# Kernel tuning notes

Measured on AMD Instinct MI355X. Metric: run time of the kernel, lower is better.

The kernel has to match this reference:

```python
import jax, jax.numpy as jnp
import numpy as np

B, L, E, H, EXP = 2, 2048, 1024, 16, 4
D = E // H
EPS = 1e-5

def layernorm(x, g, b):
    mu = jnp.mean(x, axis=-1, keepdims=True)
    var = jnp.var(x, axis=-1, keepdims=True)
    return (x - mu) * jax.lax.rsqrt(var + EPS) * g + b

def setup_inputs() -> dict:
    key = jax.random.key(0)
    ks = jax.random.split(key, 12)
    s = 0.02
    return {
        "x": jax.random.normal(ks[0], (B, L, E), dtype=jnp.float32),
        "ln1_g": jnp.ones((E,), jnp.float32),
        "ln1_b": jnp.zeros((E,), jnp.float32),
        "W_qkv": jax.random.normal(ks[1], (E, 3 * E), dtype=jnp.float32) * s,
        "W_proj": jax.random.normal(ks[2], (E, E), dtype=jnp.float32) * s,
        "b_proj": jnp.zeros((E,), jnp.float32),
        "ln2_g": jnp.ones((E,), jnp.float32),
        "ln2_b": jnp.zeros((E,), jnp.float32),
        "W1": jax.random.normal(ks[3], (E, EXP * E), dtype=jnp.float32) * s,
        "b1": jnp.zeros((EXP * E,), jnp.float32),
        "W2": jax.random.normal(ks[4], (EXP * E, E), dtype=jnp.float32) * s,
        "b2": jnp.zeros((E,), jnp.float32),
    }

def reference(x, ln1_g, ln1_b, W_qkv, W_proj, b_proj, ln2_g, ln2_b, W1, b1, W2, b2):
    # --- attention sub-block (pre-LN) ---
    h = layernorm(x, ln1_g, ln1_b)                      # [B,L,E]
    qkv = h @ W_qkv                                      # [B,L,3E]
    q, k, v = jnp.split(qkv, 3, axis=-1)
    q = q.reshape(B, L, H, D).transpose(0, 2, 1, 3)      # [B,H,L,D]
    k = k.reshape(B, L, H, D).transpose(0, 2, 1, 3)
    v = v.reshape(B, L, H, D).transpose(0, 2, 1, 3)
    scale = jnp.sqrt(jnp.float32(E))                     # NOTE: module divides by sqrt(E), not sqrt(D)
    att = jnp.einsum('bhqd,bhkd->bhqk', q, k) / scale
    att = jax.nn.softmax(att, axis=-1)
    out = jnp.einsum('bhqk,bhkd->bhqd', att, v)          # [B,H,L,D]
    out = out.transpose(0, 2, 1, 3).reshape(B, L, E)
    x = x + out @ W_proj + b_proj                         # residual
    # --- feed-forward sub-block (pre-LN) ---
    h = layernorm(x, ln2_g, ln2_b)
    h = jax.nn.gelu(h @ W1 + b1, approximate=False)       # torch GELU is exact erf
    x = x + h @ W2 + b2
    return x
```

## Files before the change

### kernel.cpp

```cpp
#include <hip/hip_runtime.h>
#include <cstdint>
#include <cstddef>


typedef __bf16 bht;
typedef __attribute__((ext_vector_type(8))) __bf16 bf16x8;
typedef __attribute__((ext_vector_type(4))) __bf16 bf16x4;
typedef __attribute__((ext_vector_type(4))) float f32x4;
typedef __attribute__((ext_vector_type(4))) short short4v;

#define B_ 2
#define L_ 2048
#define E_ 1024
#define H_ 16
#define D_ 64
#define ROWS_ (B_ * L_)

#define QSCALE_ 0.045084441f

__device__ __forceinline__ void glds16(const void* g, void* l) {
    __builtin_amdgcn_global_load_lds(
        (const __attribute__((address_space(1))) unsigned int*)g,
        (__attribute__((address_space(3))) unsigned int*)l, 16, 0, 0);
}

__device__ __forceinline__ short4v as_s4(bf16x4 v) {
    return __builtin_bit_cast(short4v, v);
}

__global__ __launch_bounds__(256)
void transpose_cast(const float* __restrict__ in, bht* __restrict__ out, int R, int C) {
    __shared__ float tile[32][33];
    const int bx = blockIdx.x * 32;
    const int by = blockIdx.y * 32;
    const int tx = threadIdx.x, ty = threadIdx.y;
    #pragma unroll
    for (int i = 0; i < 32; i += 8)
        tile[ty + i][tx] = in[(size_t)(by + ty + i) * C + bx + tx];
    __syncthreads();
    #pragma unroll
    for (int i = 0; i < 32; i += 8)
        out[(size_t)(bx + ty + i) * R + by + tx] = (bht)tile[tx][ty + i];
}

__global__ __launch_bounds__(256)
void ln_kernel(const float* __restrict__ x, const float* __restrict__ g,
               const float* __restrict__ b, bht* __restrict__ out) {
    const int row = blockIdx.x, t = threadIdx.x;
    const float4 v = ((const float4*)(x + (size_t)row * E_))[t];
    float s  = v.x + v.y + v.z + v.w;
    float ss = v.x*v.x + v.y*v.y + v.z*v.z + v.w*v.w;
    #pragma unroll
    for (int off = 32; off > 0; off >>= 1) {
        s  += __shfl_down(s, off);
        ss += __shfl_down(ss, off);
    }
    __shared__ float red[8];
    const int wave = t >> 6, lane = t & 63;
    if (lane == 0) { red[wave] = s; red[4 + wave] = ss; }
    __syncthreads();
    s  = red[0] + red[1] + red[2] + red[3];
    ss = red[4] + red[5] + red[6] + red[7];
    const float mean = s * (1.0f / (float)E_);
    const float var  = ss * (1.0f / (float)E_) - mean * mean;
    const float rstd = rsqrtf(var + 1e-5f);
    const float4 gv = ((const float4*)g)[t];
    const float4 bv = ((const float4*)b)[t];
    bf16x4 o;
    o.x = (bht)((v.x - mean) * rstd * gv.x + bv.x);
    o.y = (bht)((v.y - mean) * rstd * gv.y + bv.y);
    o.z = (bht)((v.z - mean) * rstd * gv.z + bv.z);
    o.w = (bht)((v.w - mean) * rstd * gv.w + bv.w);
    *(bf16x4*)(out + (size_t)row * E_ + t * 4) = o;
}

enum { EPI_QKV = 0, EPI_RESID = 1, EPI_GELU = 2 };

template <int EPI>
__global__ __launch_bounds__(256)
void gemm_bt(const bht* __restrict__ A, const bht* __restrict__ Bt,
             const float* __restrict__ bias, const float* __restrict__ resid,
             void* __restrict__ outp,
             bht* __restrict__ qo, bht* __restrict__ ko, bht* __restrict__ vto,
             int M, int N, int K) {
    __shared__ __align__(16) char smem[33792];
    bht* As = (bht*)smem;
    bht* Bs = (bht*)(smem + 16384);
    const int t = threadIdx.x;
    const int lane = t & 63, wave = t >> 6;
    const int lane15 = lane & 15, quad = lane >> 4;
    const int waveM = wave >> 1, waveN = wave & 1;
    const int bm = blockIdx.y * 128, bn = blockIdx.x * 128;

    f32x4 acc[4][4];
    #pragma unroll
    for (int i = 0; i < 4; ++i)
        #pragma unroll
        for (int j = 0; j < 4; ++j)
            acc[i][j] = f32x4{0.f, 0.f, 0.f, 0.f};

    const int swz = lane15 & 7;

    for (int k0 = 0; k0 < K; k0 += 64) {
        #pragma unroll
        for (int i = 0; i < 4; ++i) {
            const int g = i * 256 + t;
            const int row = g >> 3;
            const int col = ((g & 7) ^ (row & 7)) * 8;
            glds16(A  + (size_t)(bm + row) * K + k0 + col, (char*)As + (size_t)g * 16);
            glds16(Bt + (size_t)(bn + row) * K + k0 + col, (char*)Bs + (size_t)g * 16);
        }
        __syncthreads();
        #pragma unroll
        for (int kk = 0; kk < 2; ++kk) {
            const int pc = ((kk * 4 + quad) ^ swz) * 8;
            bf16x8 af[4], bfv[4];
            #pragma unroll
            for (int i = 0; i < 4; ++i)
                af[i] = *(const bf16x8*)(As + (waveM * 64 + i * 16 + lane15) * 64 + pc);
            #pragma unroll
            for (int j = 0; j < 4; ++j)
                bfv[j] = *(const bf16x8*)(Bs + (waveN * 64 + j * 16 + lane15) * 64 + pc);
            #pragma unroll
            for (int i = 0; i < 4; ++i)
                #pragma unroll
                for (int j = 0; j < 4; ++j)
                    acc[i][j] = __builtin_amdgcn_mfma_f32_16x16x32_bf16(af[i], bfv[j], acc[i][j], 0, 0, 0);
        }
        __syncthreads();
    }

    if constexpr (EPI == EPI_QKV) {
        if (bn >= 2048) {
            bht* Vtile = (bht*)smem;
            #pragma unroll
            for (int i = 0; i < 4; ++i) {
                const int rl0 = waveM * 64 + i * 16 + quad * 4;
                #pragma unroll
                for (int j = 0; j < 4; ++j) {
                    const int cl = waveN * 64 + j * 16 + lane15;
                    #pragma unroll
                    for (int r = 0; r < 4; ++r)
                        Vtile[(size_t)cl * 132 + rl0 + r] = (bht)acc[i][j][r];
                }
            }
            __syncthreads();
            const int b = bm >> 11;
            const int l0 = bm & 2047;
            #pragma unroll
            for (int it = 0; it < 8; ++it) {
                const int row = it * 16 + (t >> 4);
                const int ch  = t & 15;
                const int cg = (bn - 2048) + row;
                const int h = cg >> 6, d = cg & 63;
                const int bh = b * H_ + h;
                bf16x8 vv = *(const bf16x8*)(Vtile + (size_t)row * 132 + ch * 8);
                if (t & 128)
                    vv = __builtin_shufflevector(vv, vv, 4, 5, 6, 7, 0, 1, 2, 3);
                *(bf16x8*)(vto + ((size_t)bh * D_ + d) * L_ + l0 + ch * 8) = vv;
            }
        } else {
            #pragma unroll
            for (int i = 0; i < 4; ++i) {
                const int row0 = bm + waveM * 64 + i * 16 + quad * 4;
                #pragma unroll
                for (int j = 0; j < 4; ++j) {
                    const int col = bn + waveN * 64 + j * 16 + lane15;
                    const int seg = col >> 10;
                    const int c = col & 1023;
                    const int h = c >> 6, d = c & 63;
                    #pragma unroll
                    for (int r = 0; r < 4; ++r) {
                        const int m = row0 + r;
                        const int b = m >> 11, l = m & 2047;
                        const int bh = b * H_ + h;
                        const float v = acc[i][j][r];
                        if (seg == 0)
                            qo[((size_t)bh * L_ + l) * D_ + d] = (bht)(v * QSCALE_);
                        else
                            ko[((size_t)bh * L_ + l) * D_ + d] = (bht)v;
                    }
                }
            }
        }
    } else {
        #pragma unroll
        for (int i = 0; i < 4; ++i) {
            const int row0 = bm + waveM * 64 + i * 16 + quad * 4;
            #pragma unroll
            for (int j = 0; j < 4; ++j) {
                const int col = bn + waveN * 64 + j * 16 + lane15;
                #pragma unroll
                for (int r = 0; r < 4; ++r) {
                    const int m = row0 + r;
                    float v = acc[i][j][r];
                    if (EPI == EPI_RESID) {
                        ((float*)outp)[(size_t)m * N + col] =
                            v + bias[col] + resid[(size_t)m * N + col];
                    } else {
                        v += bias[col];
                        v = 0.5f * v * (1.0f + erff(v * 0.70710678118654752f));
                        ((bht*)outp)[(size_t)m * N + col] = (bht)v;
                    }
                }
            }
        }
    }
}

template <int EPI>
__global__ __launch_bounds__(256)
void gemm_bt64(const bht* __restrict__ A, const bht* __restrict__ Bt,
               const float* __restrict__ bias, const float* __restrict__ resid,
               void* __restrict__ outp, int M, int N, int K) {
    __shared__ __align__(16) bht As[64 * 64];
    __shared__ __align__(16) bht Bs[128 * 64];
    const int t = threadIdx.x;
    const int lane = t & 63, wave = t >> 6;
    const int lane15 = lane & 15, quad = lane >> 4;
    const int waveM = wave >> 1, waveN = wave & 1;
    const int bm = blockIdx.y * 64, bn = blockIdx.x * 128;

    f32x4 acc[2][4];
    #pragma unroll
    for (int i = 0; i < 2; ++i)
        #pragma unroll
        for (int j = 0; j < 4; ++j)
            acc[i][j] = f32x4{0.f, 0.f, 0.f, 0.f};

    const int swz = lane15 & 7;

    for (int k0 = 0; k0 < K; k0 += 64) {
        #pragma unroll
        for (int i = 0; i < 2; ++i) {
            const int g = i * 256 + t;
            const int row = g >> 3;
            const int col = ((g & 7) ^ (row & 7)) * 8;
            glds16(A + (size_t)(bm + row) * K + k0 + col, (char*)As + (size_t)g * 16);
        }
        #pragma unroll
        for (int i = 0; i < 4; ++i) {
            const int g = i * 256 + t;
            const int row = g >> 3;
            const int col = ((g & 7) ^ (row & 7)) * 8;
            glds16(Bt + (size_t)(bn + row) * K + k0 + col, (char*)Bs + (size_t)g * 16);
        }
        __syncthreads();
        #pragma unroll
        for (int kk = 0; kk < 2; ++kk) {
            const int pc = ((kk * 4 + quad) ^ swz) * 8;
            bf16x8 af[2], bfv[4];
            #pragma unroll
            for (int i = 0; i < 2; ++i)
                af[i] = *(const bf16x8*)(As + (waveM * 32 + i * 16 + lane15) * 64 + pc);
            #pragma unroll
            for (int j = 0; j < 4; ++j)
                bfv[j] = *(const bf16x8*)(Bs + (waveN * 64 + j * 16 + lane15) * 64 + pc);
            #pragma unroll
            for (int i = 0; i < 2; ++i)
                #pragma unroll
                for (int j = 0; j < 4; ++j)
                    acc[i][j] = __builtin_amdgcn_mfma_f32_16x16x32_bf16(af[i], bfv[j], acc[i][j], 0, 0, 0);
        }
        __syncthreads();
    }

    #pragma unroll
    for (int i = 0; i < 2; ++i) {
        const int row0 = bm + waveM * 32 + i * 16 + quad * 4;
        #pragma unroll
        for (int j = 0; j < 4; ++j) {
            const int col = bn + waveN * 64 + j * 16 + lane15;
            #pragma unroll
            for (int r = 0; r < 4; ++r) {
                const int m = row0 + r;
                float v = acc[i][j][r];
                if (EPI == EPI_RESID) {
                    ((float*)outp)[(size_t)m * N + col] =
                        v + bias[col] + resid[(size_t)m * N + col];
                } else {
                    v += bias[col];
                    v = 0.5f * v * (1.0f + erff(v * 0.70710678118654752f));
                    ((bht*)outp)[(size_t)m * N + col] = (bht)v;
                }
            }
        }
    }
}

#define KT_ 128
#define NT_ (L_ / KT_)

__global__ __launch_bounds__(256)
void attn_kernel(const bht* __restrict__ Q, const bht* __restrict__ Kb,
                 const bht* __restrict__ Vt, bht* __restrict__ O) {
    __shared__ __align__(16) bht Ks[KT_ * 64];
    __shared__ __align__(16) bht Vs[64 * KT_];
    __shared__ float Ls[4][16];
    const int t = threadIdx.x;
    const int lane = t & 63, wave = t >> 6;
    const int lane15 = lane & 15, quad = lane >> 4;
    const int bh = blockIdx.x, qt = blockIdx.y;

    const bht* Qh = Q  + (size_t)bh * L_ * D_;
    const bht* Kh = Kb + (size_t)bh * L_ * D_;
    const bht* Vh = Vt + (size_t)bh * D_ * L_;

    const int q0 = qt * 64 + wave * 16;

    bf16x8 aq[2];
    #pragma unroll
    for (int kc = 0; kc < 2; ++kc)
        aq[kc] = *(const bf16x8*)(Qh + (size_t)(q0 + lane15) * D_ + kc * 32 + quad * 8);

    f32x4 o_acc[4];
    #pragma unroll
    for (int db = 0; db < 4; ++db) o_acc[db] = f32x4{0.f, 0.f, 0.f, 0.f};
    float l_sum = 0.f;

    const int pc0 = (quad ^ (lane15 & 7)) * 8;
    const int pc1 = pc0 ^ 32;
    const int vhalf4 = ((quad & 1) ^ ((lane15 >> 3) & 1)) * 4;

    auto stageK = [&](int kt2) {
        const int key0 = kt2 * KT_;
        #pragma unroll
        for (int i = 0; i < 4; ++i) {
            const int g = i * 256 + t;
            const int krow = g >> 3;
            const int ksc = ((g & 7) ^ (krow & 7)) * 8;
            glds16(Kh + (size_t)(key0 + krow) * D_ + ksc, (char*)Ks + (size_t)g * 16);
        }
    };
    auto stageV = [&](int kt2) {
        const int key0 = kt2 * KT_;
        #pragma unroll
        for (int i = 0; i < 4; ++i) {
            const int g = i * 256 + t;
            const int vrow = g >> 4;
            const int vsc = ((g & 15) ^ (vrow & 7)) * 8;
            glds16(Vh + (size_t)vrow * L_ + key0 + vsc, (char*)Vs + (size_t)g * 16);
        }
    };

    stageK(0);
    stageV(0);

    for (int kt = 0; kt < NT_; ++kt) {
        asm volatile("s_waitcnt vmcnt(4) lgkmcnt(0)" ::: "memory");
        __builtin_amdgcn_s_barrier();

        __builtin_amdgcn_s_setprio(1);
        short4v pk[8];
        #pragma unroll
        for (int nb = 0; nb < 8; ++nb) {
            const bf16x8 ak0 = *(const bf16x8*)(Ks + (nb * 16 + lane15) * 64 + pc0);
            const bf16x8 ak1 = *(const bf16x8*)(Ks + (nb * 16 + lane15) * 64 + pc1);
            f32x4 st = __builtin_amdgcn_mfma_f32_16x16x32_bf16(
                ak0, aq[0], f32x4{0.f, 0.f, 0.f, 0.f}, 0, 0, 0);
            st = __builtin_amdgcn_mfma_f32_16x16x32_bf16(ak1, aq[1], st, 0, 0, 0);
            bf16x4 pkv;
            #pragma unroll
            for (int r = 0; r < 4; ++r) {
                const float pv = exp2f(st[r]);
                l_sum += pv;
                pkv[r] = (bht)pv;
            }
            pk[nb] = as_s4(pkv);
        }
        __builtin_amdgcn_s_setprio(0);

        asm volatile("s_waitcnt vmcnt(0) lgkmcnt(0)" ::: "memory");
        __builtin_amdgcn_s_barrier();
        if (kt + 1 < NT_) stageK(kt + 1);

        __builtin_amdgcn_s_setprio(1);
        #pragma unroll
        for (int nb = 0; nb < 8; ++nb) {
            #pragma unroll
            for (int db = 0; db < 4; ++db) {
                const int row = db * 16 + lane15;
                const int c16 = (nb * 2 + (quad >> 1)) ^ (row & 7);
                const bf16x4 bv = *(const bf16x4*)(Vs + row * KT_ + c16 * 8 + vhalf4);
                o_acc[db] = __builtin_amdgcn_mfma_f32_16x16x16bf16_1k(
                    pk[nb], as_s4(bv), o_acc[db], 0, 0, 0);
            }
        }
        __builtin_amdgcn_s_setprio(0);

        asm volatile("s_waitcnt lgkmcnt(0)" ::: "memory");
        __builtin_amdgcn_s_barrier();
        if (kt + 1 < NT_) stageV(kt + 1);
    }

    l_sum += __shfl_xor(l_sum, 16);
    l_sum += __shfl_xor(l_sum, 32);
    Ls[wave][lane15] = l_sum;
    asm volatile("s_waitcnt lgkmcnt(0)" ::: "memory");

    const int b = bh >> 4, h = bh & 15;
    #pragma unroll
    for (int r = 0; r < 4; ++r) {
        const int l = q0 + quad * 4 + r;
        const float inv = 1.0f / Ls[wave][quad * 4 + r];
        #pragma unroll
        for (int db = 0; db < 4; ++db)
            O[((size_t)b * L_ + l) * E_ + h * 64 + db * 16 + lane15] =
                (bht)(o_acc[db][r] * inv);
    }
}

extern "C" void kernel_launch(void* const* d_in, const int* in_sizes, int n_in,
                              void* d_out, int out_size, void* d_ws, size_t ws_size,
                              hipStream_t stream) {
    const float* x      = (const float*)d_in[0];
    const float* ln1_g  = (const float*)d_in[1];
    const float* ln1_b  = (const float*)d_in[2];
    const float* W_qkv  = (const float*)d_in[3];
    const float* W_proj = (const float*)d_in[4];
    const float* b_proj = (const float*)d_in[5];
    const float* ln2_g  = (const float*)d_in[6];
    const float* ln2_b  = (const float*)d_in[7];
    const float* W1     = (const float*)d_in[8];
    const float* b1     = (const float*)d_in[9];
    const float* W2     = (const float*)d_in[10];
    const float* b2     = (const float*)d_in[11];
    float* out = (float*)d_out;

    char* ws = (char*)d_ws;
    auto alloc = [&](size_t bytes) {
        char* p = ws;
        ws += (bytes + 255) & ~(size_t)255;
        return p;
    };
    bht*   WqkvT  = (bht*)alloc((size_t)3072 * 1024 * 2);
    bht*   WprojT = (bht*)alloc((size_t)1024 * 1024 * 2);
    bht*   W1T    = (bht*)alloc((size_t)4096 * 1024 * 2);
    bht*   W2T    = (bht*)alloc((size_t)1024 * 4096 * 2);
    bht*   hb     = (bht*)alloc((size_t)ROWS_ * E_ * 2);
    float* x1     = (float*)alloc((size_t)ROWS_ * E_ * 4);
    bht*   Qb     = (bht*)alloc((size_t)B_ * H_ * L_ * D_ * 2);
    bht*   Kbuf   = (bht*)alloc((size_t)B_ * H_ * L_ * D_ * 2);
    bht*   Vtb    = (bht*)alloc((size_t)B_ * H_ * D_ * L_ * 2);
    bht*   attno  = (bht*)alloc((size_t)ROWS_ * E_ * 2);
    bht*   ffn1   = Qb;

    transpose_cast<<<dim3(3072 / 32, 1024 / 32), dim3(32, 8), 0, stream>>>(W_qkv, WqkvT, 1024, 3072);
    transpose_cast<<<dim3(1024 / 32, 1024 / 32), dim3(32, 8), 0, stream>>>(W_proj, WprojT, 1024, 1024);
    transpose_cast<<<dim3(4096 / 32, 1024 / 32), dim3(32, 8), 0, stream>>>(W1, W1T, 1024, 4096);
    transpose_cast<<<dim3(1024 / 32, 4096 / 32), dim3(32, 8), 0, stream>>>(W2, W2T, 4096, 1024);

    ln_kernel<<<ROWS_, 256, 0, stream>>>(x, ln1_g, ln1_b, hb);

    gemm_bt<EPI_QKV><<<dim3(3072 / 128, ROWS_ / 128), 256, 0, stream>>>(
        hb, WqkvT, nullptr, nullptr, nullptr, Qb, Kbuf, Vtb, ROWS_, 3072, 1024);

    attn_kernel<<<dim3(B_ * H_, L_ / 64), 256, 0, stream>>>(Qb, Kbuf, Vtb, attno);

    gemm_bt64<EPI_RESID><<<dim3(1024 / 128, ROWS_ / 64), 256, 0, stream>>>(
        attno, WprojT, b_proj, x, x1, ROWS_, 1024, 1024);

    ln_kernel<<<ROWS_, 256, 0, stream>>>(x1, ln2_g, ln2_b, hb);

    gemm_bt<EPI_GELU><<<dim3(4096 / 128, ROWS_ / 128), 256, 0, stream>>>(
        hb, W1T, b1, nullptr, ffn1, nullptr, nullptr, nullptr, ROWS_, 4096, 1024);

    gemm_bt64<EPI_RESID><<<dim3(1024 / 128, ROWS_ / 64), 256, 0, stream>>>(
        ffn1, W2T, b2, x1, out, ROWS_, 1024, 4096);

    (void)in_sizes; (void)n_in; (void)out_size; (void)ws_size;
}
```

Baseline: 382.0 us.

## Replace 128x128 GEMM with triple-buffered 256x256 tile kernel for QKV and FFN1

Replaces the single-buffered 128x128 bf16 GEMM used for the QKV projection and the first FFN layer with a 256x256-tile, 512-thread kernel. It triple-buffers LDS over 32-wide K steps and splits each step into two MFMA phases with staged loads in between. The goal is more operand reuse per byte loaded and overlap of global-to-LDS traffic with MFMA work. The V-transpose epilogue is redone in two halves so it fits the larger tile. Separately, attention swaps exp2f for the hardware exp2 builtin. The cost is higher register and LDS pressure, and fewer blocks on the grid (192 and 256).

Result: faster. 354.7 us (-7.1%).

```diff
diff --git a/kernel.cpp b/kernel.cpp
--- a/kernel.cpp
+++ b/kernel.cpp
@@ -26,6 +26,14 @@
 
 __device__ __forceinline__ short4v as_s4(bf16x4 v) {
     return __builtin_bit_cast(short4v, v);
+}
+
+__device__ __forceinline__ float fast_exp2(float x) {
+#if __has_builtin(__builtin_amdgcn_exp2f)
+    return __builtin_amdgcn_exp2f(x);
+#else
+    return exp2f(x);
+#endif
 }
 
 __global__ __launch_bounds__(256)
@@ -77,135 +85,178 @@
 enum { EPI_QKV = 0, EPI_RESID = 1, EPI_GELU = 2 };
 
 template <int EPI>
-__global__ __launch_bounds__(256)
-void gemm_bt(const bht* __restrict__ A, const bht* __restrict__ Bt,
-             const float* __restrict__ bias, const float* __restrict__ resid,
-             void* __restrict__ outp,
+__global__ __launch_bounds__(512, 2)
+void gemm256(const bht* __restrict__ A, const bht* __restrict__ Bt,
+             const float* __restrict__ bias, void* __restrict__ outp,
              bht* __restrict__ qo, bht* __restrict__ ko, bht* __restrict__ vto,
              int M, int N, int K) {
-    __shared__ __align__(16) char smem[33792];
-    bht* As = (bht*)smem;
-    bht* Bs = (bht*)(smem + 16384);
+    __shared__ __align__(16) char smem_[98304];
     const int t = threadIdx.x;
     const int lane = t & 63, wave = t >> 6;
     const int lane15 = lane & 15, quad = lane >> 4;
-    const int waveM = wave >> 1, waveN = wave & 1;
-    const int bm = blockIdx.y * 128, bn = blockIdx.x * 128;
-
-    f32x4 acc[4][4];
-    #pragma unroll
-    for (int i = 0; i < 4; ++i)
+    const int waveM = wave >> 2, waveN = wave & 3;
+    const int bm = blockIdx.y * 256, bn = blockIdx.x * 256;
+
+    f32x4 acc[8][4];
+    #pragma unroll
+    for (int i = 0; i < 8; ++i)
         #pragma unroll
         for (int j = 0; j < 4; ++j)
             acc[i][j] = f32x4{0.f, 0.f, 0.f, 0.f};
 
-    const int swz = lane15 & 7;
-
-    for (int k0 = 0; k0 < K; k0 += 64) {
-        #pragma unroll
-        for (int i = 0; i < 4; ++i) {
-            const int g = i * 256 + t;
-            const int row = g >> 3;
-            const int col = ((g & 7) ^ (row & 7)) * 8;
-            glds16(A  + (size_t)(bm + row) * K + k0 + col, (char*)As + (size_t)g * 16);
-            glds16(Bt + (size_t)(bn + row) * K + k0 + col, (char*)Bs + (size_t)g * 16);
-        }
-        __syncthreads();
-        #pragma unroll
-        for (int kk = 0; kk < 2; ++kk) {
-            const int pc = ((kk * 4 + quad) ^ swz) * 8;
-            bf16x8 af[4], bfv[4];
-            #pragma unroll
-            for (int i = 0; i < 4; ++i)
-                af[i] = *(const bf16x8*)(As + (waveM * 64 + i * 16 + lane15) * 64 + pc);
-            #pragma unroll
-            for (int j = 0; j < 4; ++j)
-                bfv[j] = *(const bf16x8*)(Bs + (waveN * 64 + j * 16 + lane15) * 64 + pc);
-            #pragma unroll
-            for (int i = 0; i < 4; ++i)
+    const int apc = ((quad ^ (lane15 & 3)) & 3) * 8;
+    const int aoff = waveM * 4096 + lane15 * 32 + apc;
+    const int boff = waveN * 2048 + lane15 * 32 + apc;
+
+    auto stage_step = [&](int s, int op, int bufi) {
+        const int k0 = s * 32;
+        const bht* src = op ? Bt : A;
+        const int rb = op ? bn : bm;
+        char* dst = smem_ + (size_t)bufi * 32768 + op * 16384;
+        #pragma unroll
+        for (int i = 0; i < 2; ++i) {
+            const int g = i * 512 + t;
+            const int row = g >> 2;
+            const int c = ((g & 3) ^ (row & 3)) * 8;
+            glds16(src + (size_t)(rb + row) * K + k0 + c, dst + (size_t)g * 16);
+        }
+    };
+
+    const int NT = K >> 5;
+    stage_step(0, 0, 0); stage_step(0, 1, 0);
+    stage_step(1, 0, 1); stage_step(1, 1, 1);
+
+    int cb = 0;
+    for (int s = 0; s < NT; ++s) {
+        const int nb2 = (cb >= 1) ? cb - 1 : 2;
+        if (s + 2 < NT) {
+            stage_step(s + 2, 0, nb2);
+            asm volatile("s_waitcnt vmcnt(6)" ::: "memory");
+        } else if (s + 1 < NT) {
+            asm volatile("s_waitcnt vmcnt(4)" ::: "memory");
+        } else {
+            asm volatile("s_waitcnt vmcnt(0)" ::: "memory");
+        }
+        __builtin_amdgcn_s_barrier();
+        asm volatile("" ::: "memory");
+
+        const bht* Au = (const bht*)(smem_ + (size_t)cb * 32768);
+        const bht* Bu = (const bht*)(smem_ + (size_t)cb * 32768 + 16384);
+        bf16x8 af0[4], bfv[4];
+        #pragma unroll
+        for (int m = 0; m < 4; ++m)
+            af0[m] = *(const bf16x8*)(Au + aoff + m * 512);
+        #pragma unroll
+        for (int n = 0; n < 4; ++n)
+            bfv[n] = *(const bf16x8*)(Bu + boff + n * 512);
+        asm volatile("s_waitcnt lgkmcnt(0)" ::: "memory");
+        __builtin_amdgcn_s_setprio(1);
+        #pragma unroll
+        for (int m = 0; m < 4; ++m)
+            #pragma unroll
+            for (int n = 0; n < 4; ++n)
+                acc[m][n] = __builtin_amdgcn_mfma_f32_16x16x32_bf16(af0[m], bfv[n], acc[m][n], 0, 0, 0);
+        __builtin_amdgcn_s_setprio(0);
+        __builtin_amdgcn_s_barrier();
+        asm volatile("" ::: "memory");
+
+        bf16x8 af1[4];
+        #pragma unroll
+        for (int m = 0; m < 4; ++m)
+            af1[m] = *(const bf16x8*)(Au + aoff + (m + 4) * 512);
+        if (s + 2 < NT) stage_step(s + 2, 1, nb2);
+        asm volatile("s_waitcnt lgkmcnt(0)" ::: "memory");
+        __builtin_amdgcn_s_setprio(1);
+        #pragma unroll
+        for (int m = 0; m < 4; ++m)
+            #pragma unroll
+            for (int n = 0; n < 4; ++n)
+                acc[m + 4][n] = __builtin_amdgcn_mfma_f32_16x16x32_bf16(af1[m], bfv[n], acc[m + 4][n], 0, 0, 0);
+        __builtin_amdgcn_s_setprio(0);
+        __builtin_amdgcn_s_barrier();
+        asm volatile("" ::: "memory");
+
+        cb = (cb == 2) ? 0 : cb + 1;
+    }
+
+    if constexpr (EPI == EPI_GELU) {
+        #pragma unroll
+        for (int m = 0; m < 8; ++m) {
+            const int row0 = bm + waveM * 128 + m * 16 + quad * 4;
+            #pragma unroll
+            for (int n = 0; n < 4; ++n) {
+                const int col = bn + waveN * 64 + n * 16 + lane15;
                 #pragma unroll
-                for (int j = 0; j < 4; ++j)
-                    acc[i][j] = __builtin_amdgcn_mfma_f32_16x16x32_bf16(af[i], bfv[j], acc[i][j], 0, 0, 0);
-        }
-        __syncthreads();
-    }
-
-    if constexpr (EPI == EPI_QKV) {
-        if (bn >= 2048) {
-            bht* Vtile = (bht*)smem;
-            #pragma unroll
-            for (int i = 0; i < 4; ++i) {
-                const int rl0 = waveM * 64 + i * 16 + quad * 4;
-                #pragma unroll
-                for (int j = 0; j < 4; ++j) {
-                    const int cl = waveN * 64 + j * 16 + lane15;
-                    #pragma unroll
-                    for (int r = 0; r < 4; ++r)
-                        Vtile[(size_t)cl * 132 + rl0 + r] = (bht)acc[i][j][r];
+                for (int r = 0; r < 4; ++r) {
+                    float v = acc[m][n][r] + bias[col];
+                    v = 0.5f * v * (1.0f + erff(v * 0.70710678118654752f));
+                    ((bht*)outp)[(size_t)(row0 + r) * N + col] = (bht)v;
                 }
             }
-            __syncthreads();
-            const int b = bm >> 11;
-            const int l0 = bm & 2047;
-            #pragma unroll
-            for (int it = 0; it < 8; ++it) {
-                const int row = it * 16 + (t >> 4);
-                const int ch  = t & 15;
-                const int cg = (bn - 2048) + row;
-                const int h = cg >> 6, d = cg & 63;
-                const int bh = b * H_ + h;
-                bf16x8 vv = *(const bf16x8*)(Vtile + (size_t)row * 132 + ch * 8);
-                if (t & 128)
-                    vv = __builtin_shufflevector(vv, vv, 4, 5, 6, 7, 0, 1, 2, 3);
-                *(bf16x8*)(vto + ((size_t)bh * D_ + d) * L_ + l0 + ch * 8) = vv;
+        }
+    } else {
+        const int b = bm >> 11, l0 = bm & 2047;
+        if (bn >= 2048) {
+            bht* Vtile = (bht*)smem_;
+            #pragma unroll
+            for (int h = 0; h < 2; ++h) {
+                if ((waveN >> 1) == h) {
+                    #pragma unroll
+                    for (int m = 0; m < 8; ++m) {
+                        const int rl0 = waveM * 128 + m * 16 + quad * 4;
+                        #pragma unroll
+                        for (int n = 0; n < 4; ++n) {
+                            const int c = (waveN & 1) * 64 + n * 16 + lane15;
+                            #pragma unroll
+                            for (int r = 0; r < 4; ++r)
+                                Vtile[(size_t)c * 264 + rl0 + r] = (bht)acc[m][n][r];
+                        }
+                    }
+                }
+                __syncthreads();
+                #pragma unroll
+                for (int it = 0; it < 4; ++it) {
+                    const int c2 = it * 32 + (t >> 4);
+                    const int cg = (bn - 2048) + h * 128 + c2;
+                    const int hh = cg >> 6, d = cg & 63;
+                    const int bh2 = b * H_ + hh;
+                    #pragma unroll
+                    for (int half2 = 0; half2 < 2; ++half2) {
+                        const int ch = (t & 15) + 16 * half2;
+                        bf16x8 vv = *(const bf16x8*)(Vtile + (size_t)c2 * 264 + ch * 8);
+                        if (d & 8)
+                            vv = __builtin_shufflevector(vv, vv, 4, 5, 6, 7, 0, 1, 2, 3);
+                        *(bf16x8*)(vto + ((size_t)bh2 * D_ + d) * L_ + l0 + ch * 8) = vv;
+                    }
+                }
+                __syncthreads();
             }
         } else {
             #pragma unroll
-            for (int i = 0; i < 4; ++i) {
-                const int row0 = bm + waveM * 64 + i * 16 + quad * 4;
+            for (int m = 0; m < 8; ++m) {
+                const int row0 = bm + waveM * 128 + m * 16 + quad * 4;
                 #pragma unroll
-                for (int j = 0; j < 4; ++j) {
-                    const int col = bn + waveN * 64 + j * 16 + lane15;
+                for (int n = 0; n < 4; ++n) {
+                    const int col = bn + waveN * 64 + n * 16 + lane15;
                     const int seg = col >> 10;
                     const int c = col & 1023;
-                    const int h = c >> 6, d = c & 63;
+                    const int hh = c >> 6, d = c & 63;
                     #pragma unroll
                     for (int r = 0; r < 4; ++r) {
-                        const int m = row0 + r;
-                        const int b = m >> 11, l = m & 2047;
-                        const int bh = b * H_ + h;
-                        const float v = acc[i][j][r];
+                        const int mrow = row0 + r;
+                        const int bb = mrow >> 11, l = mrow & 2047;
+                        const int bh2 = bb * H_ + hh;
+                        const float v = acc[m][n][r];
                         if (seg == 0)
-                            qo[((size_t)bh * L_ + l) * D_ + d] = (bht)(v * QSCALE_);
+                            qo[((size_t)bh2 * L_ + l) * D_ + d] = (bht)(v * QSCALE_);
                         else
-                            ko[((size_t)bh * L_ + l) * D_ + d] = (bht)v;
+                            ko[((size_t)bh2 * L_ + l) * D_ + d] = (bht)v;
                     }
                 }
             }
         }
-    } else {
-        #pragma unroll
-        for (int i = 0; i < 4; ++i) {
-            const int row0 = bm + waveM * 64 + i * 16 + quad * 4;
-            #pragma unroll
-            for (int j = 0; j < 4; ++j) {
-                const int col = bn + waveN * 64 + j * 16 + lane15;
-                #pragma unroll
-                for (int r = 0; r < 4; ++r) {
-                    const int m = row0 + r;
-                    float v = acc[i][j][r];
-                    if (EPI == EPI_RESID) {
-                        ((float*)outp)[(size_t)m * N + col] =
-                            v + bias[col] + resid[(size_t)m * N + col];
-                    } else {
-                        v += bias[col];
-                        v = 0.5f * v * (1.0f + erff(v * 0.70710678118654752f));
-                        ((bht*)outp)[(size_t)m * N + col] = (bht)v;
-                    }
-                }
-            }
-        }
-    }
+    }
+    (void)M;
 }
 
 template <int EPI>
@@ -362,7 +413,7 @@
             bf16x4 pkv;
             #pragma unroll
             for (int r = 0; r < 4; ++r) {
-                const float pv = exp2f(st[r]);
+                const float pv = fast_exp2(st[r]);
                 l_sum += pv;
                 pkv[r] = (bht)pv;
             }
@@ -452,8 +503,8 @@
 
     ln_kernel<<<ROWS_, 256, 0, stream>>>(x, ln1_g, ln1_b, hb);
 
-    gemm_bt<EPI_QKV><<<dim3(3072 / 128, ROWS_ / 128), 256, 0, stream>>>(
-        hb, WqkvT, nullptr, nullptr, nullptr, Qb, Kbuf, Vtb, ROWS_, 3072, 1024);
+    gemm256<EPI_QKV><<<dim3(3072 / 256, ROWS_ / 256), 512, 0, stream>>>(
+        hb, WqkvT, nullptr, nullptr, Qb, Kbuf, Vtb, ROWS_, 3072, 1024);
 
     attn_kernel<<<dim3(B_ * H_, L_ / 64), 256, 0, stream>>>(Qb, Kbuf, Vtb, attno);
 
@@ -462,8 +513,8 @@
 
     ln_kernel<<<ROWS_, 256, 0, stream>>>(x1, ln2_g, ln2_b, hb);
 
-    gemm_bt<EPI_GELU><<<dim3(4096 / 128, ROWS_ / 128), 256, 0, stream>>>(
-        hb, W1T, b1, nullptr, ffn1, nullptr, nullptr, nullptr, ROWS_, 4096, 1024);
+    gemm256<EPI_GELU><<<dim3(4096 / 256, ROWS_ / 256), 512, 0, stream>>>(
+        hb, W1T, b1, ffn1, nullptr, nullptr, nullptr, ROWS_, 4096, 1024);
 
     gemm_bt64<EPI_RESID><<<dim3(1024 / 128, ROWS_ / 64), 256, 0, stream>>>(
         ffn1, W2T, b2, x1, out, ROWS_, 1024, 4096);
```
